# Kernel tuning notes

Measured on AMD Instinct MI355X. Metric: run time of the kernel, lower is better.

The kernel has to match this reference:

```python
import jax, jax.numpy as jnp
import numpy as np
from functools import partial

K = 3
P = K * K * K          # 27 kernel points
G = 2                  # groups
PAD = 1
STRIDE = 1
DIL = 1
AXIS_SCALE = (0.5, 1.0, 1.0)   # (x, y, z) offset axis scale
CUR_SCALE = 0.5                # warmup scale at global_step=0
EPS = 1e-5


def setup_inputs() -> dict:
    key = jax.random.key(0)
    ks = jax.random.split(key, 8)
    C, OC = 64, 64
    N, D, H, W = 1, 32, 32, 32
    inp = {
        "x": jax.random.normal(ks[0], (N, C, D, H, W), jnp.float32),
        "dw_w": jax.random.normal(ks[1], (C, 1, K, K, K), jnp.float32) * 0.1,
        "gn_w": jnp.ones((C,), jnp.float32),
        "gn_b": jnp.zeros((C,), jnp.float32),
        "inp_w": jax.random.normal(ks[2], (C, C), jnp.float32) * (1.0 / np.sqrt(C)),
        "inp_b": jnp.zeros((C,), jnp.float32),
        # offset/mask weights are zero-init in the module; use small random values
        # so the deformable sampling path is exercised nontrivially.
        "off_w": jax.random.normal(ks[3], (C, G * P * 3), jnp.float32) * 0.01,
        "off_b": jnp.zeros((G * P * 3,), jnp.float32),
        "mask_w": jax.random.normal(ks[4], (C, G * P), jnp.float32) * 0.01,
        "mask_b": jnp.tile(jnp.full((P,), -5.0, jnp.float32).at[P // 2].set(0.0), (G,)),
        "out_w": jax.random.normal(ks[5], (C, OC), jnp.float32) * (1.0 / np.sqrt(C)),
        "out_b": jnp.zeros((OC,), jnp.float32),
    }
    return inp


def _trilinear(vol, loc):
    # vol: [Dp, Hp, Wp, gc]; loc: [..., 3] with (x, y, z) in [-1, 1]
    # grid_sample semantics: align_corners=False, padding_mode='zeros'
    Dp, Hp, Wp, _ = vol.shape
    ix = (loc[..., 0] + 1.0) * 0.5 * Wp - 0.5
    iy = (loc[..., 1] + 1.0) * 0.5 * Hp - 0.5
    iz = (loc[..., 2] + 1.0) * 0.5 * Dp - 0.5
    x0f, y0f, z0f = jnp.floor(ix), jnp.floor(iy), jnp.floor(iz)
    fx, fy, fz = ix - x0f, iy - y0f, iz - z0f
    x0, y0, z0 = x0f.astype(jnp.int32), y0f.astype(jnp.int32), z0f.astype(jnp.int32)
    out = jnp.zeros(loc.shape[:-1] + (vol.shape[-1],), vol.dtype)
    for dz in (0, 1):
        wz = fz if dz else 1.0 - fz
        cz = z0 + dz
        for dy in (0, 1):
            wy = fy if dy else 1.0 - fy
            cy = y0 + dy
            for dx in (0, 1):
                wx = fx if dx else 1.0 - fx
                cx = x0 + dx
                valid = ((cz >= 0) & (cz < Dp) & (cy >= 0) & (cy < Hp)
                         & (cx >= 0) & (cx < Wp))
                v = vol[jnp.clip(cz, 0, Dp - 1),
                        jnp.clip(cy, 0, Hp - 1),
                        jnp.clip(cx, 0, Wp - 1)]  # [..., gc]
                out = out + (wz * wy * wx * valid.astype(vol.dtype))[..., None] * v
    return out


def _forward(x, dw_w, gn_w, gn_b, inp_w, inp_b, off_w, off_b,
             mask_w, mask_b, out_w, out_b):
    N, C, D, H, W = x.shape
    gc = C // G
    # --- dw_conv: depthwise conv3d + GroupNorm(1, C) + GELU ---
    xc = jax.lax.conv_general_dilated(
        x, dw_w, window_strides=(1, 1, 1), padding=[(PAD, PAD)] * 3,
        dimension_numbers=("NCDHW", "OIDHW", "NCDHW"), feature_group_count=C)
    mu = xc.mean(axis=(1, 2, 3, 4), keepdims=True)
    var = ((xc - mu) ** 2).mean(axis=(1, 2, 3, 4), keepdims=True)
    xn = (xc - mu) * jax.lax.rsqrt(var + EPS)
    xn = xn * gn_w[None, :, None, None, None] + gn_b[None, :, None, None, None]
    x1 = jnp.transpose(jax.nn.gelu(xn), (0, 2, 3, 4, 1))       # [N,D,H,W,C]
    # --- offset / mask / input projection ---
    offset = x1 @ off_w + off_b                                  # [N,D,H,W,G*P*3]
    mask = jax.nn.softmax(
        (x1 @ mask_w + mask_b).reshape(N, D, H, W, G, P), axis=-1)
    xp = jnp.transpose(x, (0, 2, 3, 4, 1)) @ inp_w + inp_b       # [N,D,H,W,C]
    # --- core deformable sampling ---
    x_pad = jnp.pad(xp, ((0, 0), (PAD, PAD), (PAD, PAD), (PAD, PAD), (0, 0)))
    Dp, Hp, Wp = D + 2 * PAD, H + 2 * PAD, W + 2 * PAD
    Do = (D + 2 * PAD - DIL * (K - 1) - 1) // STRIDE + 1
    Ho = (H + 2 * PAD - DIL * (K - 1) - 1) // STRIDE + 1
    Wo = (W + 2 * PAD - DIL * (K - 1) - 1) // STRIDE + 1
    # reference grid (x/Wp, y/Hp, z/Dp)
    zc, yc, xc_ = jnp.meshgrid(jnp.arange(Do, dtype=jnp.float32),
                               jnp.arange(Ho, dtype=jnp.float32),
                               jnp.arange(Wo, dtype=jnp.float32), indexing="ij")
    ref = jnp.stack(((xc_ * STRIDE + PAD + 0.5) / Wp,
                     (yc * STRIDE + PAD + 0.5) / Hp,
                     (zc * STRIDE + PAD + 0.5) / Dp), axis=-1)   # [Do,Ho,Wo,3]
    # kernel grid
    lin = jnp.linspace(-(K - 1) // 2, (K - 1) // 2, K, dtype=jnp.float32)
    kz, ky, kx = jnp.meshgrid(lin, lin, lin, indexing="ij")
    kgrid = jnp.stack((kx * DIL / Wp, ky * DIL / Hp, kz * DIL / Dp),
                      axis=-1).reshape(P, 3)
    off = offset.reshape(N, Do, Ho, Wo, G, P, 3)
    off_norm = off / jnp.array([Wp, Hp, Dp], jnp.float32)
    axis = jnp.array(AXIS_SCALE, jnp.float32)
    loc = (ref[None, :, :, :, None, None, :]
           + kgrid[None, None, None, None, None, :, :]
           + off_norm * axis * CUR_SCALE)
    loc = loc * 2.0 - 1.0                                        # [N,Do,Ho,Wo,G,P,3]
    vol = jnp.transpose(x_pad.reshape(N, Dp, Hp, Wp, G, gc),
                        (0, 4, 1, 2, 3, 5))                      # [N,G,Dp,Hp,Wp,gc]
    locs = jnp.transpose(loc, (0, 4, 1, 2, 3, 5, 6))             # [N,G,Do,Ho,Wo,P,3]
    sampled = jax.vmap(jax.vmap(_trilinear))(vol, locs)          # [N,G,Do,Ho,Wo,P,gc]
    out = jnp.einsum("ngdhwpc,ndhwgp->ndhwgc", sampled, mask)
    out = out.reshape(N, Do, Ho, Wo, C)
    return out @ out_w + out_b                                   # [N,Do,Ho,Wo,OC]


def reference(x, dw_w, gn_w, gn_b, inp_w, inp_b, off_w, off_b,
              mask_w, mask_b, out_w, out_b):
    return _forward(x, dw_w, gn_w, gn_b, inp_w, inp_b, off_w, off_b,
                    mask_w, mask_b, out_w, out_b)
```

## Files before the change

### kernel.cpp

```cpp
#include <hip/hip_runtime.h>
#include <hip/hip_fp16.h>
#include <math.h>

#define SP 32768
#define PW 38
#define PW2 (PW*PW)
#define PVOX (PW*PW*PW)
#define OMS 228

typedef short bf16x8 __attribute__((ext_vector_type(8)));
typedef unsigned short u16x4 __attribute__((ext_vector_type(4)));
typedef float f32x4 __attribute__((ext_vector_type(4)));

__device__ __forceinline__ unsigned short f2b(float f) {
    unsigned u = __float_as_uint(f);
    u = (u + 0x7FFFu + ((u >> 16) & 1u)) >> 16;
    return (unsigned short)u;
}
__device__ __forceinline__ float b2f1(unsigned short s) {
    return __uint_as_float(((unsigned)s) << 16);
}
__device__ __forceinline__ __half2 h2(unsigned u) {
    return *reinterpret_cast<__half2*>(&u);
}
__device__ __forceinline__ int vox_of(int sb, int v) {
    int tw = sb & 7, th = (sb >> 3) & 15, td = sb >> 7;
    int vw = v & 3, vh = (v >> 2) & 1, vd = v >> 3;
    return (((td << 1) + vd) << 10) + (((th << 1) + vh) << 5) + (tw << 2) + vw;
}

__global__ void k_front(const float* __restrict__ x, const float* __restrict__ dw,
                        const float* __restrict__ off_w, const float* __restrict__ mask_w,
                        const float* __restrict__ off_b, const float* __restrict__ mask_b,
                        const float* __restrict__ inp_w, const float* __restrict__ out_w,
                        unsigned short* __restrict__ WcatB, float* __restrict__ bcat,
                        unsigned short* __restrict__ inpB, unsigned short* __restrict__ outB,
                        unsigned short* __restrict__ x_tb,
                        unsigned short* __restrict__ xcb, float* __restrict__ partials,
                        unsigned short* __restrict__ xpad) {
    int bb = blockIdx.x, tid = threadIdx.x;
    if (bb < 88) {
        int idx = bb * 256 + tid;
        int j = idx >> 6, k = idx & 63;
        if (j < 224) {
            float v = 0.f;
            if (j < 162) v = off_w[k * 162 + j];
            else if (j < 216) v = mask_w[k * 54 + (j - 162)];
            WcatB[j * 64 + k] = f2b(v);
            if (k == 0) bcat[j] = (j < 162) ? off_b[j] : (j < 216 ? mask_b[j - 162] : 0.f);
        } else if (j < 288) {
            outB[(j - 224) * 64 + k] = f2b(out_w[k * 64 + (j - 224)]);
        } else {
            inpB[(j - 288) * 64 + k] = f2b(inp_w[k * 64 + (j - 288)]);
        }
        return;
    }
    if (bb < 600) {
        __shared__ unsigned short tile[64][66];
        int s0 = (bb - 88) * 64;
        int row = tid >> 6, lane = tid & 63;
        for (int c = row; c < 64; c += 4)
            tile[c][lane] = f2b(x[(size_t)c * SP + s0 + lane]);
        __syncthreads();
        for (int r = row; r < 64; r += 4)
            x_tb[(size_t)(s0 + r) * 64 + lane] = tile[lane][r];
        return;
    }
    if (bb < 2648) {
        int b4 = bb - 600;
        int e4 = b4 * 256 + tid;
        int c = e4 >> 13, s4 = (e4 & 8191) << 2;
        int d = s4 >> 10, h = (s4 >> 5) & 31, w0 = s4 & 31;
        const float* xs = x + (size_t)c * SP;
        const float* wt = dw + c * 27;
        float a0 = 0.f, a1 = 0.f, a2 = 0.f, a3 = 0.f;
#pragma unroll
        for (int kd = 0; kd < 3; ++kd) {
            int zz = d + kd - 1; if ((unsigned)zz >= 32u) continue;
#pragma unroll
            for (int kh = 0; kh < 3; ++kh) {
                int yy = h + kh - 1; if ((unsigned)yy >= 32u) continue;
                const float* row = xs + (zz << 10) + (yy << 5) + w0;
                float4 L = *(const float4*)row;
                float xl = (w0 > 0) ? row[-1] : 0.f;
                float xr = (w0 < 28) ? row[4] : 0.f;
                const float* wr = wt + kd * 9 + kh * 3;
                float wm = wr[0], wc = wr[1], wp = wr[2];
                a0 = __builtin_fmaf(wm, xl,  __builtin_fmaf(wc, L.x, __builtin_fmaf(wp, L.y, a0)));
                a1 = __builtin_fmaf(wm, L.x, __builtin_fmaf(wc, L.y, __builtin_fmaf(wp, L.z, a1)));
                a2 = __builtin_fmaf(wm, L.y, __builtin_fmaf(wc, L.z, __builtin_fmaf(wp, L.w, a2)));
                a3 = __builtin_fmaf(wm, L.z, __builtin_fmaf(wc, L.w, __builtin_fmaf(wp, xr,  a3)));
            }
        }
        u16x4 o4; o4[0] = f2b(a0); o4[1] = f2b(a1); o4[2] = f2b(a2); o4[3] = f2b(a3);
        *(u16x4*)(xcb + (size_t)e4 * 4) = o4;
        __shared__ float rs[256], rq[256];
        rs[tid] = a0 + a1 + a2 + a3;
        rq[tid] = a0 * a0 + a1 * a1 + a2 * a2 + a3 * a3;
        __syncthreads();
        for (int off = 128; off > 0; off >>= 1) {
            if (tid < off) { rs[tid] += rs[tid + off]; rq[tid] += rq[tid + off]; }
            __syncthreads();
        }
        if (tid == 0) {
            partials[b4 * 2 + 0] = rs[0];
            partials[b4 * 2 + 1] = rq[0];
        }
        return;
    }
    int cblk = bb - 2648;
    int j = tid >> 4, c4 = tid & 15;
    u16x4 z = {0, 0, 0, 0};
#pragma unroll
    for (int k = 0; k < 4; ++k) {
        int v = cblk * 64 + k * 16 + j;
        if (v >= PVOX) break;
        int zz = v / PW2, r = v - zz * PW2, yy = r / PW, xx = r - yy * PW;
        if (zz < 2 || zz > 33 || yy < 2 || yy > 33 || xx < 2 || xx > 33)
            *(u16x4*)(xpad + (size_t)v * 64 + c4 * 4) = z;
    }
}

__global__ void k_mid(const unsigned short* __restrict__ xcb, const float* __restrict__ partials,
                      const float* __restrict__ gn_w, const float* __restrict__ gn_b,
                      unsigned short* __restrict__ x1b,
                      const unsigned short* __restrict__ x_tb,
                      const unsigned short* __restrict__ inpB,
                      const float* __restrict__ inp_b,
                      unsigned short* __restrict__ xpad) {
    int bb = blockIdx.x, tid = threadIdx.x;
    if (bb < 512) {
        __shared__ float rs[256], rq[256];
        __shared__ unsigned short tile[64][66];
        float a = 0.f, b = 0.f;
        for (int i = tid; i < 2048; i += 256) { a += partials[2 * i]; b += partials[2 * i + 1]; }
        rs[tid] = a; rq[tid] = b;
        __syncthreads();
        for (int off = 128; off > 0; off >>= 1) {
            if (tid < off) { rs[tid] += rs[tid + off]; rq[tid] += rq[tid + off]; }
            __syncthreads();
        }
        const float Minv = 1.f / 2097152.f;
        float mu = rs[0] * Minv;
        float var = rq[0] * Minv - mu * mu;
        float rsq = rsqrtf(var + 1e-5f);
        int s0 = bb * 64;
        int row = tid >> 6, lane = tid & 63;
        for (int c = row; c < 64; c += 4) {
            float v = (b2f1(xcb[(size_t)c * SP + s0 + lane]) - mu) * rsq * gn_w[c] + gn_b[c];
            float t2 = 1.5957691216057308f * (v + 0.044715f * v * v * v);
            tile[c][lane] = f2b(v / (1.f + __expf(-t2)));
        }
        __syncthreads();
        for (int r = row; r < 64; r += 4)
            x1b[(size_t)(s0 + r) * 64 + lane] = tile[lane][r];
        return;
    }
    {
        int wv = tid >> 6, lane = tid & 63;
        int quad = lane >> 4, col = lane & 15;
        int s0 = (bb - 512) * 64 + wv * 16;
        bf16x8 a0 = *(const bf16x8*)(x_tb + (size_t)(s0 + col) * 64 + quad * 8);
        bf16x8 a1 = *(const bf16x8*)(x_tb + (size_t)(s0 + col) * 64 + 32 + quad * 8);
        int vp[4];
#pragma unroll
        for (int r = 0; r < 4; ++r) {
            int s = s0 + (quad << 2) + r;
            vp[r] = (((s >> 10) + 2) * PW + ((s >> 5) & 31) + 2) * PW + (s & 31) + 2;
        }
#pragma unroll
        for (int nt = 0; nt < 4; ++nt) {
            int n0 = nt * 16;
            bf16x8 b0 = *(const bf16x8*)(inpB + (n0 + col) * 64 + quad * 8);
            bf16x8 b1 = *(const bf16x8*)(inpB + (n0 + col) * 64 + 32 + quad * 8);
            f32x4 c = {0.f, 0.f, 0.f, 0.f};
            c = __builtin_amdgcn_mfma_f32_16x16x32_bf16(a0, b0, c, 0, 0, 0);
            c = __builtin_amdgcn_mfma_f32_16x16x32_bf16(a1, b1, c, 0, 0, 0);
            float bq = inp_b[n0 + col];
#pragma unroll
            for (int r = 0; r < 4; ++r)
                xpad[(size_t)vp[r] * 64 + n0 + col] =
                    __half_as_ushort(__float2half(c[r] + bq));
        }
    }
}

__device__ __forceinline__ void sample27_lds(const float* __restrict__ orow,
                                             const float* __restrict__ mrow,
                                             const char* __restrict__ volp,
                                             float xb, float yb, float zb,
                                             float* __restrict__ acc) {
#pragma unroll
    for (int p = 0; p < 27; ++p) {
        const int px = p % 3, py = (p / 3) % 3, pz = p / 9;
        float ox = orow[p * 3 + 0], oy = orow[p * 3 + 1], oz = orow[p * 3 + 2];
        float mk = mrow[p];
        float ix = __builtin_fmaf(0.25f, ox, xb + (float)px);
        float iy = __builtin_fmaf(0.5f, oy, yb + (float)py);
        float iz = __builtin_fmaf(0.5f, oz, zb + (float)pz);
        ix = fminf(fmaxf(ix, 0.f), 6.999f);
        iy = fminf(fmaxf(iy, 0.f), 4.999f);
        iz = fminf(fmaxf(iz, 0.f), 4.999f);
        float xf = floorf(ix), yf = floorf(iy), zf = floorf(iz);
        float fx = ix - xf, fy = iy - yf, fz = iz - zf;
        float fi = __builtin_fmaf(zf, 48.f, __builtin_fmaf(yf, 8.f, xf));
        int rr = (int)fi;
        #define RD(o) (*(const uint4*)(volp + ((rr + (o)) << 7)))
        uint4 r000 = RD(0);
        uint4 r001 = RD(1);
        uint4 r010 = RD(8);
        uint4 r011 = RD(9);
        uint4 r100 = RD(48);
        uint4 r101 = RD(49);
        uint4 r110 = RD(56);
        uint4 r111 = RD(57);
        #undef RD
        __half2 fx2 = __float2half2_rn(fx);
        __half2 fy2 = __float2half2_rn(fy);
        __half2 fz2 = __float2half2_rn(fz);
        #define TRI(comp, ci)                                                   \
        {                                                                       \
            __half2 t0 = __hfma2(fx2, __hsub2(h2(r001.comp), h2(r000.comp)), h2(r000.comp)); \
            __half2 t1 = __hfma2(fx2, __hsub2(h2(r011.comp), h2(r010.comp)), h2(r010.comp)); \
            __half2 t2 = __hfma2(fx2, __hsub2(h2(r101.comp), h2(r100.comp)), h2(r100.comp)); \
            __half2 t3 = __hfma2(fx2, __hsub2(h2(r111.comp), h2(r110.comp)), h2(r110.comp)); \
            __half2 u0 = __hfma2(fy2, __hsub2(t1, t0), t0);                     \
            __half2 u1 = __hfma2(fy2, __hsub2(t3, t2), t2);                     \
            __half2 rr2 = __hfma2(fz2, __hsub2(u1, u0), u0);                    \
            float2 ff = __half22float2(rr2);                                    \
            acc[2 * ci + 0] = __builtin_fmaf(mk, ff.x, acc[2 * ci + 0]);        \
            acc[2 * ci + 1] = __builtin_fmaf(mk, ff.y, acc[2 * ci + 1]);        \
        }
        TRI(x, 0) TRI(y, 1) TRI(z, 2) TRI(w, 3)
        #undef TRI
    }
}

__global__ void __launch_bounds__(128, 2) k_main(const unsigned short* __restrict__ x1b,
                                                 const unsigned short* __restrict__ xpad,
                                                 const unsigned short* __restrict__ WcatB,
                                                 const float* __restrict__ bcat,
                                                 const unsigned short* __restrict__ outB,
                                                 const float* __restrict__ out_b,
                                                 float* __restrict__ out) {
    __shared__ float om_s[16 * OMS];
    __shared__ unsigned short smb[16 * 72];
    __shared__ char vol[288 * 128];
    int tid = threadIdx.x, wv = tid >> 6, lane = tid & 63;
    int quad = lane >> 4, col = lane & 15;
    int sb = ((blockIdx.x & 7) << 8) | (blockIdx.x >> 3);
    int tw = sb & 7, th = (sb >> 3) & 15, td = sb >> 7;
    {
        const char* xp = (const char*)xpad;
#pragma unroll
        for (int k = 0; k < 3; ++k) {
            uint4 t[6];
#pragma unroll
            for (int j = 0; j < 6; ++j) {
                int u = tid + (k * 6 + j) * 128;
                int rr = u >> 3, ch = u & 7;
                int dz = rr / 48, rem = rr - dz * 48, dy = rem >> 3, dx = rem & 7;
                int pv = ((2 * td + dz) * PW + (2 * th + dy)) * PW + 4 * tw + dx;
                t[j] = *(const uint4*)(xp + ((size_t)pv << 7) + (ch << 4));
            }
#pragma unroll
            for (int j = 0; j < 6; ++j) {
                int u = tid + (k * 6 + j) * 128;
                *(uint4*)(vol + (u << 4)) = t[j];
            }
        }
    }
    {
        int sv = vox_of(sb, col);
        bf16x8 a0 = *(const bf16x8*)(x1b + (size_t)sv * 64 + quad * 8);
        bf16x8 a1 = *(const bf16x8*)(x1b + (size_t)sv * 64 + 32 + quad * 8);
        for (int jt = wv; jt < 14; jt += 2) {
            int n0 = jt * 16;
            bf16x8 b0 = *(const bf16x8*)(WcatB + (n0 + col) * 64 + quad * 8);
            bf16x8 b1 = *(const bf16x8*)(WcatB + (n0 + col) * 64 + 32 + quad * 8);
            f32x4 c = {0.f, 0.f, 0.f, 0.f};
            c = __builtin_amdgcn_mfma_f32_16x16x32_bf16(a0, b0, c, 0, 0, 0);
            c = __builtin_amdgcn_mfma_f32_16x16x32_bf16(a1, b1, c, 0, 0, 0);
            float bb = bcat[n0 + col];
            int n = n0 + col, slot;
            if (n < 162) slot = n + ((n >= 81) ? 3 : 0);
            else { int n2 = n - 162; slot = 168 + n2 + ((n2 >= 27) ? 1 : 0); }
            if (n < 216) {
#pragma unroll
                for (int r = 0; r < 4; ++r)
                    om_s[(quad * 4 + r) * OMS + slot] = c[r] + bb;
            }
        }
    }
    __syncthreads();
    {
        int row = lane >> 2, sub = lane & 3;
        int vloc = wv * 8 + (row >> 1), g = row & 1;
        float* m = &om_s[vloc * OMS + 168 + g * 28];
        float mv[7];
        float mx = -1e30f;
#pragma unroll
        for (int i = 0; i < 7; ++i) {
            int p = sub * 7 + i;
            mv[i] = (p < 27) ? m[p] : -1e30f;
            mx = fmaxf(mx, mv[i]);
        }
        mx = fmaxf(mx, __shfl_xor(mx, 1));
        mx = fmaxf(mx, __shfl_xor(mx, 2));
        float e[7], sm = 0.f;
#pragma unroll
        for (int i = 0; i < 7; ++i) { e[i] = __expf(mv[i] - mx); sm += e[i]; }
        sm += __shfl_xor(sm, 1);
        sm += __shfl_xor(sm, 2);
        float inv = 1.f / sm;
#pragma unroll
        for (int i = 0; i < 7; ++i) {
            int p = sub * 7 + i;
            if (p < 27) m[p] = e[i] * inv;
        }
    }
    {
        int v = wv * 8 + (lane >> 3);
        int oct = lane & 7, gg = oct >> 2;
        int vw = v & 3, vh = (v >> 2) & 1, vd = v >> 3;
        float xb = (float)(vw + 1);
        float yb = (float)(vh + 1);
        float zb = (float)(vd + 1);
        const float* orow = &om_s[v * OMS + gg * 84];
        const float* mrow = &om_s[v * OMS + 168 + gg * 28];
        float acc[8] = {0.f, 0.f, 0.f, 0.f, 0.f, 0.f, 0.f, 0.f};
        sample27_lds(orow, mrow, vol + oct * 16, xb, yb, zb, acc);
        bf16x8 sb8;
#pragma unroll
        for (int k = 0; k < 8; ++k) sb8[k] = (short)f2b(acc[k]);
        *(bf16x8*)(smb + v * 72 + oct * 8) = sb8;
    }
    __syncthreads();
    {
        bf16x8 oa0 = *(const bf16x8*)(smb + col * 72 + quad * 8);
        bf16x8 oa1 = *(const bf16x8*)(smb + col * 72 + 32 + quad * 8);
        int vr[4];
#pragma unroll
        for (int r = 0; r < 4; ++r) vr[r] = vox_of(sb, quad * 4 + r);
#pragma unroll
        for (int t = 0; t < 2; ++t) {
            int n0 = (wv + t * 2) * 16;
            bf16x8 b0 = *(const bf16x8*)(outB + (n0 + col) * 64 + quad * 8);
            bf16x8 b1 = *(const bf16x8*)(outB + (n0 + col) * 64 + 32 + quad * 8);
            f32x4 c = {0.f, 0.f, 0.f, 0.f};
            c = __builtin_amdgcn_mfma_f32_16x16x32_bf16(oa0, b0, c, 0, 0, 0);
            c = __builtin_amdgcn_mfma_f32_16x16x32_bf16(oa1, b1, c, 0, 0, 0);
            float bb = out_b[n0 + col];
#pragma unroll
            for (int r = 0; r < 4; ++r)
                out[(size_t)vr[r] * 64 + n0 + col] = c[r] + bb;
        }
    }
}

extern "C" void kernel_launch(void* const* d_in, const int* in_sizes, int n_in,
                              void* d_out, int out_size, void* d_ws, size_t ws_size,
                              hipStream_t stream) {
    const float* x      = (const float*)d_in[0];
    const float* dw_w   = (const float*)d_in[1];
    const float* gn_w   = (const float*)d_in[2];
    const float* gn_b   = (const float*)d_in[3];
    const float* inp_w  = (const float*)d_in[4];
    const float* inp_b  = (const float*)d_in[5];
    const float* off_w  = (const float*)d_in[6];
    const float* off_b  = (const float*)d_in[7];
    const float* mask_w = (const float*)d_in[8];
    const float* mask_b = (const float*)d_in[9];
    const float* out_w  = (const float*)d_in[10];
    const float* out_b  = (const float*)d_in[11];

    char* B = (char*)d_ws;
    float*          partials = (float*)(B + 256);
    unsigned short* xcb      = (unsigned short*)(B + 65792);
    unsigned short* x1b      = (unsigned short*)(B + 8454400);
    unsigned short* x_tb     = (unsigned short*)(B + 12648704);
    unsigned short* xpad     = (unsigned short*)(B + 16843008);
    unsigned short* WcatB    = (unsigned short*)(B + 30890240);
    float*          bcat     = (float*)(B + 30918912);
    unsigned short* inpB     = (unsigned short*)(B + 30919936);
    unsigned short* outB     = (unsigned short*)(B + 30928128);
    float* out = (float*)d_out;

    k_front<<<88 + 512 + 2048 + 858, 256, 0, stream>>>(x, dw_w, off_w, mask_w, off_b, mask_b,
                                                       inp_w, out_w, WcatB, bcat, inpB, outB,
                                                       x_tb, xcb, partials, xpad);
    k_mid<<<512 + 512, 256, 0, stream>>>(xcb, partials, gn_w, gn_b, x1b,
                                         x_tb, inpB, inp_b, xpad);
    k_main<<<2048, 128, 0, stream>>>(x1b, xpad, WcatB, bcat, outB, out_b, out);
}
```

Measured before the change: 156.5 us.

## Split deformable sampling across two wave pairs with global and LDS paths

```diff
diff --git a/kernel.cpp b/kernel.cpp
--- a/kernel.cpp
+++ b/kernel.cpp
@@ -185,19 +185,79 @@
     }
 }
 
-__device__ __forceinline__ void sample27_lds(const float* __restrict__ orow,
-                                             const float* __restrict__ mrow,
-                                             const char* __restrict__ volp,
-                                             float xb, float yb, float zb,
-                                             float* __restrict__ acc) {
-#pragma unroll
-    for (int p = 0; p < 27; ++p) {
+template<int P0, int NP>
+__device__ __forceinline__ void sampleN(const float* __restrict__ orow,
+                                        const float* __restrict__ mrow,
+                                        const char* __restrict__ volc,
+                                        float xb, float yb, float zb,
+                                        float* __restrict__ acc) {
+#pragma unroll
+    for (int i = 0; i < NP; ++i) {
+        const int p = P0 + i;
         const int px = p % 3, py = (p / 3) % 3, pz = p / 9;
         float ox = orow[p * 3 + 0], oy = orow[p * 3 + 1], oz = orow[p * 3 + 2];
         float mk = mrow[p];
         float ix = __builtin_fmaf(0.25f, ox, xb + (float)px);
         float iy = __builtin_fmaf(0.5f, oy, yb + (float)py);
         float iz = __builtin_fmaf(0.5f, oz, zb + (float)pz);
+        ix = fminf(fmaxf(ix, 0.f), 36.f);
+        iy = fminf(fmaxf(iy, 0.f), 36.f);
+        iz = fminf(fmaxf(iz, 0.f), 36.f);
+        float xf = floorf(ix), yf = floorf(iy), zf = floorf(iz);
+        float fx = ix - xf, fy = iy - yf, fz = iz - zf;
+        float fi = __builtin_fmaf(zf, (float)PW2, __builtin_fmaf(yf, (float)PW, xf));
+        int ib = ((int)fi) << 7;
+        const char* base = volc + ib;
+        uint4 r000 = *(const uint4*)(base);
+        uint4 r001 = *(const uint4*)(base + 128);
+        uint4 r010 = *(const uint4*)(base + PW * 128);
+        uint4 r011 = *(const uint4*)(base + PW * 128 + 128);
+        uint4 r100 = *(const uint4*)(base + PW2 * 128);
+        uint4 r101 = *(const uint4*)(base + PW2 * 128 + 128);
+        uint4 r110 = *(const uint4*)(base + (PW2 + PW) * 128);
+        uint4 r111 = *(const uint4*)(base + (PW2 + PW) * 128 + 128);
+        __half2 fx2 = __float2half2_rn(fx);
+        __half2 fy2 = __float2half2_rn(fy);
+        __half2 fz2 = __float2half2_rn(fz);
+        #define TRI(comp, ci)                                                   \
+        {                                                                       \
+            __half2 t0 = __hfma2(fx2, __hsub2(h2(r001.comp), h2(r000.comp)), h2(r000.comp)); \
+            __half2 t1 = __hfma2(fx2, __hsub2(h2(r011.comp), h2(r010.comp)), h2(r010.comp)); \
+            __half2 t2 = __hfma2(fx2, __hsub2(h2(r101.comp), h2(r100.comp)), h2(r100.comp)); \
+            __half2 t3 = __hfma2(fx2, __hsub2(h2(r111.comp), h2(r110.comp)), h2(r110.comp)); \
+            __half2 u0 = __hfma2(fy2, __hsub2(t1, t0), t0);                     \
+            __half2 u1 = __hfma2(fy2, __hsub2(t3, t2), t2);                     \
+            __half2 rr = __hfma2(fz2, __hsub2(u1, u0), u0);                     \
+            float2 ff = __half22float2(rr);                                     \
+            acc[2 * ci + 0] = __builtin_fmaf(mk, ff.x, acc[2 * ci + 0]);        \
+            acc[2 * ci + 1] = __builtin_fmaf(mk, ff.y, acc[2 * ci + 1]);        \
+        }
+        TRI(x, 0) TRI(y, 1) TRI(z, 2) TRI(w, 3)
+        #undef TRI
+    }
+}
+
+template<int P0, int NP>
+__device__ __forceinline__ void sampleL(const float* __restrict__ orow,
+                                        const float* __restrict__ mrow,
+                                        const char* __restrict__ volp,
+                                        float xb, float yb, float zb,
+                                        float* __restrict__ acc) {
+    float ox[NP], oy[NP], oz[NP], mk[NP];
+#pragma unroll
+    for (int i = 0; i < NP; ++i) {
+        ox[i] = orow[(P0 + i) * 3 + 0];
+        oy[i] = orow[(P0 + i) * 3 + 1];
+        oz[i] = orow[(P0 + i) * 3 + 2];
+        mk[i] = mrow[P0 + i];
+    }
+#pragma unroll
+    for (int i = 0; i < NP; ++i) {
+        const int p = P0 + i;
+        const int px = p % 3, py = (p / 3) % 3, pz = p / 9;
+        float ix = __builtin_fmaf(0.25f, ox[i], xb + (float)px);
+        float iy = __builtin_fmaf(0.5f, oy[i], yb + (float)py);
+        float iz = __builtin_fmaf(0.5f, oz[i], zb + (float)pz);
         ix = fminf(fmaxf(ix, 0.f), 6.999f);
         iy = fminf(fmaxf(iy, 0.f), 4.999f);
         iz = fminf(fmaxf(iz, 0.f), 4.999f);
@@ -218,6 +278,7 @@
         __half2 fx2 = __float2half2_rn(fx);
         __half2 fy2 = __float2half2_rn(fy);
         __half2 fz2 = __float2half2_rn(fz);
+        float m = mk[i];
         #define TRI(comp, ci)                                                   \
         {                                                                       \
             __half2 t0 = __hfma2(fx2, __hsub2(h2(r001.comp), h2(r000.comp)), h2(r000.comp)); \
@@ -228,15 +289,15 @@
             __half2 u1 = __hfma2(fy2, __hsub2(t3, t2), t2);                     \
             __half2 rr2 = __hfma2(fz2, __hsub2(u1, u0), u0);                    \
             float2 ff = __half22float2(rr2);                                    \
-            acc[2 * ci + 0] = __builtin_fmaf(mk, ff.x, acc[2 * ci + 0]);        \
-            acc[2 * ci + 1] = __builtin_fmaf(mk, ff.y, acc[2 * ci + 1]);        \
+            acc[2 * ci + 0] = __builtin_fmaf(m, ff.x, acc[2 * ci + 0]);         \
+            acc[2 * ci + 1] = __builtin_fmaf(m, ff.y, acc[2 * ci + 1]);         \
         }
         TRI(x, 0) TRI(y, 1) TRI(z, 2) TRI(w, 3)
         #undef TRI
     }
 }
 
-__global__ void __launch_bounds__(128, 2) k_main(const unsigned short* __restrict__ x1b,
+__global__ void __launch_bounds__(256, 2) k_main(const unsigned short* __restrict__ x1b,
                                                  const unsigned short* __restrict__ xpad,
                                                  const unsigned short* __restrict__ WcatB,
                                                  const float* __restrict__ bcat,
@@ -246,6 +307,7 @@
     __shared__ float om_s[16 * OMS];
     __shared__ unsigned short smb[16 * 72];
     __shared__ char vol[288 * 128];
+    __shared__ float pbuf[16 * 64];
     int tid = threadIdx.x, wv = tid >> 6, lane = tid & 63;
     int quad = lane >> 4, col = lane & 15;
     int sb = ((blockIdx.x & 7) << 8) | (blockIdx.x >> 3);
@@ -254,18 +316,18 @@
         const char* xp = (const char*)xpad;
 #pragma unroll
         for (int k = 0; k < 3; ++k) {
-            uint4 t[6];
-#pragma unroll
-            for (int j = 0; j < 6; ++j) {
-                int u = tid + (k * 6 + j) * 128;
+            uint4 t[3];
+#pragma unroll
+            for (int j = 0; j < 3; ++j) {
+                int u = tid + (k * 3 + j) * 256;
                 int rr = u >> 3, ch = u & 7;
                 int dz = rr / 48, rem = rr - dz * 48, dy = rem >> 3, dx = rem & 7;
                 int pv = ((2 * td + dz) * PW + (2 * th + dy)) * PW + 4 * tw + dx;
                 t[j] = *(const uint4*)(xp + ((size_t)pv << 7) + (ch << 4));
             }
 #pragma unroll
-            for (int j = 0; j < 6; ++j) {
-                int u = tid + (k * 6 + j) * 128;
+            for (int j = 0; j < 3; ++j) {
+                int u = tid + (k * 3 + j) * 256;
                 *(uint4*)(vol + (u << 4)) = t[j];
             }
         }
@@ -274,7 +336,7 @@
         int sv = vox_of(sb, col);
         bf16x8 a0 = *(const bf16x8*)(x1b + (size_t)sv * 64 + quad * 8);
         bf16x8 a1 = *(const bf16x8*)(x1b + (size_t)sv * 64 + 32 + quad * 8);
-        for (int jt = wv; jt < 14; jt += 2) {
+        for (int jt = wv; jt < 14; jt += 4) {
             int n0 = jt * 16;
             bf16x8 b0 = *(const bf16x8*)(WcatB + (n0 + col) * 64 + quad * 8);
             bf16x8 b1 = *(const bf16x8*)(WcatB + (n0 + col) * 64 + 32 + quad * 8);
@@ -295,7 +357,7 @@
     __syncthreads();
     {
         int row = lane >> 2, sub = lane & 3;
-        int vloc = wv * 8 + (row >> 1), g = row & 1;
+        int vloc = (wv & 1) * 8 + (row >> 1), g = row & 1;
         float* m = &om_s[vloc * OMS + 168 + g * 28];
         float mv[7];
         float mx = -1e30f;
@@ -320,41 +382,52 @@
         }
     }
     {
-        int v = wv * 8 + (lane >> 3);
+        int half = wv & 1, mode = wv >> 1;
+        int v = half * 8 + (lane >> 3);
         int oct = lane & 7, gg = oct >> 2;
-        int vw = v & 3, vh = (v >> 2) & 1, vd = v >> 3;
-        float xb = (float)(vw + 1);
-        float yb = (float)(vh + 1);
-        float zb = (float)(vd + 1);
         const float* orow = &om_s[v * OMS + gg * 84];
         const float* mrow = &om_s[v * OMS + 168 + gg * 28];
         float acc[8] = {0.f, 0.f, 0.f, 0.f, 0.f, 0.f, 0.f, 0.f};
-        sample27_lds(orow, mrow, vol + oct * 16, xb, yb, zb, acc);
-        bf16x8 sb8;
-#pragma unroll
-        for (int k = 0; k < 8; ++k) sb8[k] = (short)f2b(acc[k]);
-        *(bf16x8*)(smb + v * 72 + oct * 8) = sb8;
+        if (mode == 0) {
+            int sv = vox_of(sb, v);
+            float zb = (float)((sv >> 10) + 1);
+            float yb = (float)(((sv >> 5) & 31) + 1);
+            float xb = (float)((sv & 31) + 1);
+            sampleN<0, 9>(orow, mrow, (const char*)xpad + oct * 16, xb, yb, zb, acc);
+        } else {
+            int vw = v & 3, vh = (v >> 2) & 1, vd = v >> 3;
+            sampleL<9, 18>(orow, mrow, vol + oct * 16,
+                           (float)(vw + 1), (float)(vh + 1), (float)(vd + 1), acc);
+            float* pp = &pbuf[v * 64 + oct * 8];
+            *(f32x4*)(pp) = *(f32x4*)(acc);
+            *(f32x4*)(pp + 4) = *(f32x4*)(acc + 4);
+        }
+        __syncthreads();
+        if (mode == 0) {
+            const float* pp = &pbuf[v * 64 + oct * 8];
+            bf16x8 sb8;
+#pragma unroll
+            for (int k = 0; k < 8; ++k) sb8[k] = (short)f2b(acc[k] + pp[k]);
+            *(bf16x8*)(smb + v * 72 + oct * 8) = sb8;
+        }
     }
     __syncthreads();
     {
         bf16x8 oa0 = *(const bf16x8*)(smb + col * 72 + quad * 8);
         bf16x8 oa1 = *(const bf16x8*)(smb + col * 72 + 32 + quad * 8);
+        int n0 = wv * 16;
+        bf16x8 b0 = *(const bf16x8*)(outB + (n0 + col) * 64 + quad * 8);
+        bf16x8 b1 = *(const bf16x8*)(outB + (n0 + col) * 64 + 32 + quad * 8);
+        f32x4 c = {0.f, 0.f, 0.f, 0.f};
+        c = __builtin_amdgcn_mfma_f32_16x16x32_bf16(oa0, b0, c, 0, 0, 0);
+        c = __builtin_amdgcn_mfma_f32_16x16x32_bf16(oa1, b1, c, 0, 0, 0);
+        float bb = out_b[n0 + col];
         int vr[4];
 #pragma unroll
         for (int r = 0; r < 4; ++r) vr[r] = vox_of(sb, quad * 4 + r);
 #pragma unroll
-        for (int t = 0; t < 2; ++t) {
-            int n0 = (wv + t * 2) * 16;
-            bf16x8 b0 = *(const bf16x8*)(outB + (n0 + col) * 64 + quad * 8);
-            bf16x8 b1 = *(const bf16x8*)(outB + (n0 + col) * 64 + 32 + quad * 8);
-            f32x4 c = {0.f, 0.f, 0.f, 0.f};
-            c = __builtin_amdgcn_mfma_f32_16x16x32_bf16(oa0, b0, c, 0, 0, 0);
-            c = __builtin_amdgcn_mfma_f32_16x16x32_bf16(oa1, b1, c, 0, 0, 0);
-            float bb = out_b[n0 + col];
-#pragma unroll
-            for (int r = 0; r < 4; ++r)
-                out[(size_t)vr[r] * 64 + n0 + col] = c[r] + bb;
-        }
+        for (int r = 0; r < 4; ++r)
+            out[(size_t)vr[r] * 64 + n0 + col] = c[r] + bb;
     }
 }
 
@@ -391,5 +464,5 @@
                                                        x_tb, xcb, partials, xpad);
     k_mid<<<512 + 512, 256, 0, stream>>>(xcb, partials, gn_w, gn_b, x1b,
                                          x_tb, inpB, inp_b, xpad);
-    k_main<<<2048, 128, 0, stream>>>(x1b, xpad, WcatB, bcat, outB, out_b, out);
-}
+    k_main<<<2048, 256, 0, stream>>>(x1b, xpad, WcatB, bcat, outB, out_b, out);
+}
```

New measurement: 152.8 us. 2.4% less time.
